# Optimization experiments

Measured on AMD Instinct MI355X. Metric: run time of the kernel, lower is better.

## Reference

```python
import jax, jax.numpy as jnp
import numpy as np

B, L, D, V, T = 4, 512, 2048, 32000, 1024


def setup_inputs() -> dict:
    key = jax.random.key(0)
    k1, k2, k3 = jax.random.split(key, 3)
    encoder_outs = jax.random.normal(k1, (B, L, D), dtype=jnp.float32)
    embed_weight = jax.random.normal(k2, (V, D), dtype=jnp.float32) * 0.02
    input_ids = jax.random.randint(k3, (B, T), 0, V)
    # encoder (audio) tokens occupy the prefix of the LLM input sequence
    modality_mask = jnp.broadcast_to(jnp.arange(T) < L, (B, T))
    return {
        "encoder_outs": encoder_outs,
        "embed_weight": embed_weight,
        "input_ids": input_ids,
        "modality_mask": modality_mask,
    }


def reference(encoder_outs, embed_weight, input_ids, modality_mask):
    # chunked matmul in torch == one big contraction: (B,L,D) x (V,D) -> (B,L,V)
    sim = jnp.einsum("bld,vd->blv", encoder_outs, embed_weight)
    enc_norm = jnp.sqrt(jnp.sum(jnp.square(encoder_outs), axis=-1, keepdims=True))
    w_norm = jnp.sqrt(jnp.sum(jnp.square(embed_weight), axis=-1))  # (V,)
    cosine = sim / enc_norm / w_norm[None, None, :]
    quantize_index = jnp.argmax(cosine, axis=-1)  # (B, L)
    enc_quant = embed_weight[quantize_index]      # (B, L, D) gather lookup

    inputs_embeds = embed_weight[input_ids]       # (B, T, D)
    # pad encoder tokens to full sequence length, then blend via modality mask
    enc_pad = jnp.pad(enc_quant, ((0, 0), (0, T - L), (0, 0)))
    blended = jnp.where(modality_mask[:, :, None], enc_pad, inputs_embeds)
    return blended, quantize_index
```

## Files before the change

### kernel.cpp

```cpp
#include <hip/hip_runtime.h>
#include <math.h>

typedef __attribute__((ext_vector_type(8))) short short8v;
typedef __attribute__((ext_vector_type(4))) float f32x4;
typedef unsigned long long u64;
typedef unsigned short ushort_t;

constexpr int Bb = 4;
constexpr int Ll = 512;
constexpr int Dk = 2048;
constexpr int Vv = 32000;
constexpr int Tt = 1024;
constexpr int Mrows = Bb * Ll;

constexpr int BM = 256;
constexpr int BN = 256;
constexpr int BK = 64;
constexpr int NKT = Dk / BK;
constexpr int NBX = Mrows / BM;
constexpr int NBY = Vv / BN;
constexpr int NWG = NBX * NBY;
constexpr int CHUNK = NWG / 8;

constexpr int KCAND = 8;
constexpr int CAND_STRIDE = 500;

constexpr int FBM = 128;
constexpr int FBN = 128;
constexpr int FNVB = Vv / FBN;

constexpr size_t WS_NEEDED = 147914752ull;

__device__ __forceinline__ unsigned int fkey(float f) {
    unsigned int u = __float_as_uint(f);
    return (u & 0x80000000u) ? ~u : (u | 0x80000000u);
}
__device__ __forceinline__ void top2(u64& b1, u64& b2, u64 p) {
    if (p > b1) { b2 = b1; b1 = p; }
    else if (p > b2) { b2 = p; }
}
__device__ __forceinline__ u64 shfl64(u64 x, int m) {
    unsigned lo = __shfl_xor((unsigned)x, m, 64);
    unsigned hi = __shfl_xor((unsigned)(x >> 32), m, 64);
    return ((u64)hi << 32) | lo;
}
__device__ __forceinline__ ushort_t bftrunc(float x) {
    return (ushort_t)(__float_as_uint(x) >> 16);
}
__device__ __forceinline__ void gload_lds16(const void* g, void* l) {
    __builtin_amdgcn_global_load_lds(
        (const __attribute__((address_space(1))) unsigned int*)g,
        (__attribute__((address_space(3))) unsigned int*)l, 16, 0, 0);
}

__global__ __launch_bounds__(256) void convertA_kernel(const float* __restrict__ A,
                                                       ushort_t* __restrict__ Ab) {
    int i = blockIdx.x * blockDim.x + threadIdx.x;
    const float4* src = (const float4*)A;
    float4 x = src[i * 2], y = src[i * 2 + 1];
    ushort_t o[8] = {bftrunc(x.x), bftrunc(x.y), bftrunc(x.z), bftrunc(x.w),
                     bftrunc(y.x), bftrunc(y.y), bftrunc(y.z), bftrunc(y.w)};
    *(int4*)(Ab + (size_t)i * 8) = *(const int4*)o;
}

__global__ __launch_bounds__(256) void convertW_kernel(const float* __restrict__ W,
                                                       ushort_t* __restrict__ Wb,
                                                       float* __restrict__ winv) {
    int wave = (blockIdx.x * blockDim.x + threadIdx.x) >> 6;
    int lane = threadIdx.x & 63;
    if (wave >= Vv) return;
    const float4* row = (const float4*)(W + (size_t)wave * Dk);
    ushort4* orow = (ushort4*)(Wb + (size_t)wave * Dk);
    float s = 0.f;
#pragma unroll
    for (int i = 0; i < Dk / 4 / 64; ++i) {
        float4 v = row[lane + 64 * i];
        s = fmaf(v.x, v.x, s); s = fmaf(v.y, v.y, s);
        s = fmaf(v.z, v.z, s); s = fmaf(v.w, v.w, s);
        ushort4 o;
        o.x = bftrunc(v.x); o.y = bftrunc(v.y);
        o.z = bftrunc(v.z); o.w = bftrunc(v.w);
        orow[lane + 64 * i] = o;
    }
#pragma unroll
    for (int off = 32; off; off >>= 1) s += __shfl_down(s, off, 64);
    if (lane == 0) winv[wave] = 1.0f / sqrtf(s);
}

__global__ __launch_bounds__(256) void wnorm_kernel(const float* __restrict__ W,
                                                    float* __restrict__ winv) {
    int wave = (blockIdx.x * blockDim.x + threadIdx.x) >> 6;
    int lane = threadIdx.x & 63;
    if (wave >= Vv) return;
    const float4* row = (const float4*)(W + (size_t)wave * Dk);
    float s = 0.f;
#pragma unroll
    for (int i = 0; i < Dk / 4 / 64; ++i) {
        float4 v = row[lane + 64 * i];
        s = fmaf(v.x, v.x, s); s = fmaf(v.y, v.y, s);
        s = fmaf(v.z, v.z, s); s = fmaf(v.w, v.w, s);
    }
#pragma unroll
    for (int off = 32; off; off >>= 1) s += __shfl_down(s, off, 64);
    if (lane == 0) winv[wave] = 1.0f / sqrtf(s);
}

__global__ void init_best_kernel(u64* __restrict__ best) {
    int i = blockIdx.x * blockDim.x + threadIdx.x;
    if (i < Mrows) best[i] = 0ull;
}

__global__ __launch_bounds__(512, 2) void score_topk_kernel(
    const ushort_t* __restrict__ Ab, const ushort_t* __restrict__ Wb,
    const float* __restrict__ winv, u64* __restrict__ cand) {
    __shared__ __align__(16) ushort_t Alds[2][16384];
    __shared__ __align__(16) ushort_t Wlds[2][16384];

    const int orig = blockIdx.x;
    const int swz = (orig & 7) * CHUNK + (orig >> 3);
    const int bx = swz & (NBX - 1);
    const int by = swz >> 3;
    const int row0 = bx * BM;
    const int v0 = by * BN;

    const int tid = threadIdx.x;
    const int lane = tid & 63;
    const int w = tid >> 6;
    const int wr = w >> 2;
    const int wc = w & 3;

    const int rsub = lane & 15;
    const int ksub = (lane >> 4) * 8;

    const ushort_t* srcA[4];
    const ushort_t* srcW[4];
#pragma unroll
    for (int q = 0; q < 4; ++q) {
        const int fb = w * 4 + q, sub = fb >> 1, kk = fb & 1;
        srcA[q] = Ab + (size_t)(row0 + sub * 16 + rsub) * Dk + kk * 32 + ksub;
        srcW[q] = Wb + (size_t)(v0 + sub * 16 + rsub) * Dk + kk * 32 + ksub;
    }

    auto stage = [&](int buf, int t) {
        const int k0 = t * BK;
#pragma unroll
        for (int q = 0; q < 4; ++q) {
            const int fb = w * 4 + q;
            gload_lds16(srcA[q] + k0, &Alds[buf][fb * 512]);
            gload_lds16(srcW[q] + k0, &Wlds[buf][fb * 512]);
        }
    };

    f32x4 acc[8][4];
#pragma unroll
    for (int i = 0; i < 8; ++i)
#pragma unroll
        for (int j = 0; j < 4; ++j) acc[i][j] = (f32x4){0.f, 0.f, 0.f, 0.f};

    stage(0, 0);
    __syncthreads();
    int cur = 0;
    for (int t = 0; t < NKT; ++t) {
        if (t + 1 < NKT) stage(cur ^ 1, t + 1);
        const short8v* Ap = (const short8v*)&Alds[cur][0];
        const short8v* Wp = (const short8v*)&Wlds[cur][0];
#pragma unroll
        for (int kk = 0; kk < 2; ++kk) {
            short8v a[8], b[4];
#pragma unroll
            for (int mf = 0; mf < 8; ++mf)
                a[mf] = Ap[((wr * 8 + mf) * 2 + kk) * 64 + lane];
#pragma unroll
            for (int nf = 0; nf < 4; ++nf)
                b[nf] = Wp[((wc * 4 + nf) * 2 + kk) * 64 + lane];
            __builtin_amdgcn_s_setprio(1);
#pragma unroll
            for (int mf = 0; mf < 8; ++mf)
#pragma unroll
                for (int nf = 0; nf < 4; ++nf)
                    acc[mf][nf] = __builtin_amdgcn_mfma_f32_16x16x32_bf16(
                        a[mf], b[nf], acc[mf][nf], 0, 0, 0);
            __builtin_amdgcn_s_setprio(0);
        }
        __syncthreads();
        cur ^= 1;
    }

    const int cb = lane & 15;
    float wv[4];
#pragma unroll
    for (int nf = 0; nf < 4; ++nf) wv[nf] = winv[v0 + wc * 64 + nf * 16 + cb];

    u64(*red)[8] = (u64(*)[8]) & Alds[0][0];
#pragma unroll
    for (int mf = 0; mf < 8; ++mf) {
#pragma unroll
        for (int reg = 0; reg < 4; ++reg) {
            u64 b1 = 0, b2 = 0;
#pragma unroll
            for (int nf = 0; nf < 4; ++nf) {
                float s = acc[mf][nf][reg] * wv[nf];
                int v = v0 + wc * 64 + nf * 16 + cb;
                u64 p = ((u64)fkey(s) << 32) | (unsigned)(Vv - 1 - v);
                top2(b1, b2, p);
            }
#pragma unroll
            for (int m = 1; m < 16; m <<= 1) {
                u64 o1 = shfl64(b1, m);
                u64 o2 = shfl64(b2, m);
                top2(b1, b2, o1);
                top2(b1, b2, o2);
            }
            if (cb == 0) {
                int rl = wr * 128 + mf * 16 + ((lane >> 4) << 2) + reg;
                red[rl][wc * 2] = b1;
                red[rl][wc * 2 + 1] = b2;
            }
        }
    }
    __syncthreads();
    if (tid < BM) {
        u64 b1 = red[tid][0], b2 = red[tid][1];
#pragma unroll
        for (int j = 2; j < 8; ++j) top2(b1, b2, red[tid][j]);
        u64* c = cand + (size_t)(row0 + tid) * CAND_STRIDE + by * 2;
        c[0] = b1;
        c[1] = b2;
    }
}

template <typename LdsT>
__device__ __forceinline__ void topk_epilogue_f(f32x4 (&acc)[4][4], LdsT* ldsbase,
                                                const float* __restrict__ winv,
                                                u64* __restrict__ cand, int row0, int v0,
                                                int vby, int tid, int lane, int wr,
                                                int wc) {
    const int cbase = v0 + wc * 64 + (lane & 15);
    float wv[4];
#pragma unroll
    for (int nf = 0; nf < 4; ++nf) wv[nf] = winv[cbase + nf * 16];

    u64(*red)[4] = (u64(*)[4])ldsbase;
#pragma unroll
    for (int mf = 0; mf < 4; ++mf) {
#pragma unroll
        for (int reg = 0; reg < 4; ++reg) {
            u64 b1 = 0, b2 = 0;
#pragma unroll
            for (int nf = 0; nf < 4; ++nf) {
                float s = acc[mf][nf][reg] * wv[nf];
                int v = cbase + nf * 16;
                u64 p = ((u64)fkey(s) << 32) | (unsigned)(Vv - 1 - v);
                top2(b1, b2, p);
            }
#pragma unroll
            for (int m = 1; m < 16; m <<= 1) {
                u64 o1 = shfl64(b1, m);
                u64 o2 = shfl64(b2, m);
                top2(b1, b2, o1);
                top2(b1, b2, o2);
            }
            if ((lane & 15) == 0) {
                int rl = wr * 64 + mf * 16 + ((lane >> 4) << 2) + reg;
                red[rl][wc * 2] = b1;
                red[rl][wc * 2 + 1] = b2;
            }
        }
    }
    __syncthreads();
    if (tid < FBM) {
        u64 b1 = red[tid][0], b2 = red[tid][1];
        top2(b1, b2, red[tid][2]);
        top2(b1, b2, red[tid][3]);
        u64* c = cand + (size_t)(row0 + tid) * CAND_STRIDE + vby * 2;
        c[0] = b1;
        c[1] = b2;
    }
}

__global__ __launch_bounds__(256) void score_topk_fallback(
    const float* __restrict__ A, const float* __restrict__ W,
    const float* __restrict__ winv, u64* __restrict__ cand) {
    __shared__ __align__(16) short Albuf[4096];
    __shared__ __align__(16) short Wlbuf[4096];

    const int tid = threadIdx.x;
    const int row0 = blockIdx.x * FBM;
    const int v0 = blockIdx.y * FBN;
    const int lane = tid & 63;
    const int wid = tid >> 6;
    const int wr = wid >> 1, wc = wid & 1;

    const int rA = ((tid >> 6) << 4) + (tid & 15);
    const int kk = ((tid >> 4) & 3) * 8;

    const float* pa = A + (size_t)(row0 + rA) * Dk + kk;
    const float* pw = W + (size_t)(v0 + rA) * Dk + kk;

    float4 fa0, fa1, fa2, fa3, fw0, fw1, fw2, fw3;
    auto ld4 = [](const float* p) { return *(const float4*)p; };
    auto load_regs = [&](int k0) {
        fa0 = ld4(pa + k0); fa1 = ld4(pa + k0 + 4);
        fa2 = ld4(pa + k0 + (size_t)64 * Dk); fa3 = ld4(pa + k0 + (size_t)64 * Dk + 4);
        fw0 = ld4(pw + k0); fw1 = ld4(pw + k0 + 4);
        fw2 = ld4(pw + k0 + (size_t)64 * Dk); fw3 = ld4(pw + k0 + (size_t)64 * Dk + 4);
    };
    auto pk = [](float lo, float hi) {
        return (int)((__float_as_uint(lo) >> 16) | (__float_as_uint(hi) & 0xFFFF0000u));
    };
    auto cv = [&](float4 a, float4 b) {
        int4 r; r.x = pk(a.x, a.y); r.y = pk(a.z, a.w);
        r.z = pk(b.x, b.y); r.w = pk(b.z, b.w); return r;
    };
    auto write_lds = [&]() {
        *(int4*)(Albuf + tid * 8) = cv(fa0, fa1);
        *(int4*)(Albuf + tid * 8 + 2048) = cv(fa2, fa3);
        *(int4*)(Wlbuf + tid * 8) = cv(fw0, fw1);
        *(int4*)(Wlbuf + tid * 8 + 2048) = cv(fw2, fw3);
    };

    f32x4 acc[4][4];
#pragma unroll
    for (int i = 0; i < 4; ++i)
#pragma unroll
        for (int j = 0; j < 4; ++j) acc[i][j] = (f32x4){0.f, 0.f, 0.f, 0.f};

    load_regs(0);
    for (int kt = 0; kt < Dk / 32; ++kt) {
        write_lds();
        __syncthreads();
        if (kt + 1 < Dk / 32) load_regs((kt + 1) * 32);
        short8v af[4], bf[4];
        const short8v* Ap = (const short8v*)Albuf;
        const short8v* Wp = (const short8v*)Wlbuf;
#pragma unroll
        for (int mf = 0; mf < 4; ++mf) af[mf] = Ap[(wr * 4 + mf) * 64 + lane];
#pragma unroll
        for (int nf = 0; nf < 4; ++nf) bf[nf] = Wp[(wc * 4 + nf) * 64 + lane];
#pragma unroll
        for (int mf = 0; mf < 4; ++mf)
#pragma unroll
            for (int nf = 0; nf < 4; ++nf)
                acc[mf][nf] = __builtin_amdgcn_mfma_f32_16x16x32_bf16(
                    af[mf], bf[nf], acc[mf][nf], 0, 0, 0);
        __syncthreads();
    }

    topk_epilogue_f(acc, Albuf, winv, cand, row0, v0, blockIdx.y, tid, lane, wr, wc);
}

__global__ __launch_bounds__(256) void topk_kernel(const u64* __restrict__ cand,
                                                   int* __restrict__ sel, int nents) {
    int row = blockIdx.x * 4 + (threadIdx.x >> 6);
    int lane = threadIdx.x & 63;
    if (row >= Mrows) return;
    const u64* c = cand + (size_t)row * CAND_STRIDE;
    u64 v[8];
#pragma unroll
    for (int i = 0; i < 8; ++i) {
        int idx = lane + i * 64;
        v[i] = (idx < nents) ? c[idx] : 0ull;
    }
#pragma unroll
    for (int it = 0; it < KCAND; ++it) {
        u64 lm = 0;
#pragma unroll
        for (int i = 0; i < 8; ++i) lm = v[i] > lm ? v[i] : lm;
#pragma unroll
        for (int m = 32; m; m >>= 1) {
            u64 o = shfl64(lm, m);
            lm = o > lm ? o : lm;
        }
#pragma unroll
        for (int i = 0; i < 8; ++i)
            if (v[i] == lm) v[i] = 0;
        if (lane == 0) sel[row * KCAND + it] = Vv - 1 - (int)(unsigned)(lm & 0xFFFFFFFFu);
    }
}

__global__ __launch_bounds__(256) void rescore_kernel(
    const float* __restrict__ A, const float* __restrict__ W,
    const float* __restrict__ winv, const int* __restrict__ sel,
    u64* __restrict__ best) {
    int gw = (int)((blockIdx.x * blockDim.x + threadIdx.x) >> 6);
    int lane = threadIdx.x & 63;
    if (gw >= Mrows * KCAND) return;
    int row = gw >> 3, c = gw & 7;
    int v = sel[row * KCAND + c];
    const float4* a = (const float4*)(A + (size_t)row * Dk);
    const float4* w = (const float4*)(W + (size_t)v * Dk);
    float s = 0.f;
#pragma unroll
    for (int i = 0; i < Dk / 4 / 64; ++i) {
        float4 x = a[lane + 64 * i], y = w[lane + 64 * i];
        s = fmaf(x.x, y.x, s); s = fmaf(x.y, y.y, s);
        s = fmaf(x.z, y.z, s); s = fmaf(x.w, y.w, s);
    }
#pragma unroll
    for (int m = 32; m; m >>= 1) s += __shfl_xor(s, m, 64);
    if (lane == 0) {
        u64 p = ((u64)fkey(s * winv[v]) << 32) | (unsigned)(Vv - 1 - v);
        atomicMax(best + row, p);
    }
}

__global__ __launch_bounds__(256) void blend_kernel(
    const float* __restrict__ emb, const int* __restrict__ ids,
    const u64* __restrict__ best, float* __restrict__ out) {
    int row = blockIdx.x;
    int b = row / Tt;
    int t = row % Tt;
    int idx;
    if (t < Ll) {
        idx = Vv - 1 - (int)(best[b * Ll + t] & 0xFFFFFFFFu);
    } else {
        idx = ids[row];
    }
    const float4* src = (const float4*)(emb + (size_t)idx * Dk);
    float4* dst = (float4*)(out + (size_t)row * Dk);
    for (int i = threadIdx.x; i < Dk / 4; i += blockDim.x) dst[i] = src[i];
    if (t < Ll && threadIdx.x == 0) {
        out[(size_t)Bb * Tt * Dk + (size_t)(b * Ll + t)] = (float)idx;
    }
}

extern "C" void kernel_launch(void* const* d_in, const int* in_sizes, int n_in,
                              void* d_out, int out_size, void* d_ws, size_t ws_size,
                              hipStream_t stream) {
    const float* encoder_outs = (const float*)d_in[0];
    const float* embed_weight = (const float*)d_in[1];
    const int* input_ids = (const int*)d_in[2];

    float* out = (float*)d_out;

    float* winv = (float*)d_ws;
    u64* best = (u64*)((char*)d_ws + 131072);
    int* sel = (int*)((char*)d_ws + 147456);
    u64* cand = (u64*)((char*)d_ws + 262144);
    ushort_t* Abf = (ushort_t*)((char*)d_ws + 8454144);
    ushort_t* Wbf = (ushort_t*)((char*)d_ws + 16842752);

    init_best_kernel<<<(Mrows + 255) / 256, 256, 0, stream>>>(best);

    if (ws_size >= WS_NEEDED) {
        convertA_kernel<<<Mrows * Dk / 8 / 256, 256, 0, stream>>>(encoder_outs, Abf);
        convertW_kernel<<<Vv * 64 / 256, 256, 0, stream>>>(embed_weight, Wbf, winv);
        score_topk_kernel<<<NWG, 512, 0, stream>>>(Abf, Wbf, winv, cand);
        topk_kernel<<<Mrows / 4, 256, 0, stream>>>(cand, sel, 2 * NBY);
    } else {
        wnorm_kernel<<<Vv * 64 / 256, 256, 0, stream>>>(embed_weight, winv);
        dim3 grid(Mrows / FBM, Vv / FBN);
        score_topk_fallback<<<grid, 256, 0, stream>>>(encoder_outs, embed_weight, winv,
                                                      cand);
        topk_kernel<<<Mrows / 4, 256, 0, stream>>>(cand, sel, 2 * FNVB);
    }
    rescore_kernel<<<Mrows * KCAND / 4, 256, 0, stream>>>(encoder_outs, embed_weight,
                                                          winv, sel, best);
    blend_kernel<<<Bb * Tt, 256, 0, stream>>>(embed_weight, input_ids, best, out);
}
```

Baseline: 1.116 ms.

## Switch score GEMM to 32x32x16 MFMA with BK=32 staging

The score/top-k GEMM kernel moves from 16x16x32 bf16 MFMAs to 32x32x16 MFMAs, with each wave computing 4x2 tiles of 32x32. The K tile is halved to 32, which halves LDS use per block and changes the global-to-LDS staging layout. The epilogue is reworked to the 32x32 accumulator layout, with a wider 32-lane shuffle reduction. Larger MFMAs need fewer LDS fragment reads per flop, but halving BK doubles the number of K iterations and barriers.

```diff
diff --git a/kernel.cpp b/kernel.cpp
--- a/kernel.cpp
+++ b/kernel.cpp
@@ -3,6 +3,7 @@
 
 typedef __attribute__((ext_vector_type(8))) short short8v;
 typedef __attribute__((ext_vector_type(4))) float f32x4;
+typedef __attribute__((ext_vector_type(16))) float f32x16;
 typedef unsigned long long u64;
 typedef unsigned short ushort_t;
 
@@ -15,7 +16,7 @@
 
 constexpr int BM = 256;
 constexpr int BN = 256;
-constexpr int BK = 64;
+constexpr int BK = 32;
 constexpr int NKT = Dk / BK;
 constexpr int NBX = Mrows / BM;
 constexpr int NBY = Vv / BN;
@@ -113,8 +114,8 @@
 __global__ __launch_bounds__(512, 2) void score_topk_kernel(
     const ushort_t* __restrict__ Ab, const ushort_t* __restrict__ Wb,
     const float* __restrict__ winv, u64* __restrict__ cand) {
-    __shared__ __align__(16) ushort_t Alds[2][16384];
-    __shared__ __align__(16) ushort_t Wlds[2][16384];
+    __shared__ __align__(16) ushort_t Alds[2][8192];
+    __shared__ __align__(16) ushort_t Wlds[2][8192];
 
     const int orig = blockIdx.x;
     const int swz = (orig & 7) * CHUNK + (orig >> 3);
@@ -128,91 +129,84 @@
     const int w = tid >> 6;
     const int wr = w >> 2;
     const int wc = w & 3;
-
-    const int rsub = lane & 15;
-    const int ksub = (lane >> 4) * 8;
-
-    const ushort_t* srcA[4];
-    const ushort_t* srcW[4];
-#pragma unroll
-    for (int q = 0; q < 4; ++q) {
-        const int fb = w * 4 + q, sub = fb >> 1, kk = fb & 1;
-        srcA[q] = Ab + (size_t)(row0 + sub * 16 + rsub) * Dk + kk * 32 + ksub;
-        srcW[q] = Wb + (size_t)(v0 + sub * 16 + rsub) * Dk + kk * 32 + ksub;
-    }
+    const int l31 = lane & 31;
+    const int l5 = lane >> 5;
+
+    const ushort_t* sA = Ab + (size_t)(row0 + w * 32 + l31) * Dk + l5 * 8;
+    const ushort_t* sW = Wb + (size_t)(v0 + w * 32 + l31) * Dk + l5 * 8;
+
+    f32x16 acc[4][2];
+#pragma unroll
+    for (int i = 0; i < 4; ++i)
+#pragma unroll
+        for (int j = 0; j < 2; ++j)
+#pragma unroll
+            for (int r = 0; r < 16; ++r) acc[i][j][r] = 0.f;
 
     auto stage = [&](int buf, int t) {
         const int k0 = t * BK;
-#pragma unroll
-        for (int q = 0; q < 4; ++q) {
-            const int fb = w * 4 + q;
-            gload_lds16(srcA[q] + k0, &Alds[buf][fb * 512]);
-            gload_lds16(srcW[q] + k0, &Wlds[buf][fb * 512]);
-        }
+        gload_lds16(sA + k0, &Alds[buf][(2 * w) * 512]);
+        gload_lds16(sA + k0 + 16, &Alds[buf][(2 * w + 1) * 512]);
+        gload_lds16(sW + k0, &Wlds[buf][(2 * w) * 512]);
+        gload_lds16(sW + k0 + 16, &Wlds[buf][(2 * w + 1) * 512]);
     };
-
-    f32x4 acc[8][4];
-#pragma unroll
-    for (int i = 0; i < 8; ++i)
-#pragma unroll
-        for (int j = 0; j < 4; ++j) acc[i][j] = (f32x4){0.f, 0.f, 0.f, 0.f};
 
     stage(0, 0);
     __syncthreads();
+
     int cur = 0;
     for (int t = 0; t < NKT; ++t) {
         if (t + 1 < NKT) stage(cur ^ 1, t + 1);
         const short8v* Ap = (const short8v*)&Alds[cur][0];
         const short8v* Wp = (const short8v*)&Wlds[cur][0];
-#pragma unroll
-        for (int kk = 0; kk < 2; ++kk) {
-            short8v a[8], b[4];
-#pragma unroll
-            for (int mf = 0; mf < 8; ++mf)
-                a[mf] = Ap[((wr * 8 + mf) * 2 + kk) * 64 + lane];
-#pragma unroll
-            for (int nf = 0; nf < 4; ++nf)
-                b[nf] = Wp[((wc * 4 + nf) * 2 + kk) * 64 + lane];
-            __builtin_amdgcn_s_setprio(1);
-#pragma unroll
-            for (int mf = 0; mf < 8; ++mf)
-#pragma unroll
-                for (int nf = 0; nf < 4; ++nf)
-                    acc[mf][nf] = __builtin_amdgcn_mfma_f32_16x16x32_bf16(
+        __builtin_amdgcn_s_setprio(1);
+#pragma unroll
+        for (int c = 0; c < 2; ++c) {
+            short8v a[4], b[2];
+#pragma unroll
+            for (int mf = 0; mf < 4; ++mf)
+                a[mf] = Ap[((wr * 4 + mf) * 2 + c) * 64 + lane];
+#pragma unroll
+            for (int nf = 0; nf < 2; ++nf)
+                b[nf] = Wp[((wc * 2 + nf) * 2 + c) * 64 + lane];
+#pragma unroll
+            for (int mf = 0; mf < 4; ++mf)
+#pragma unroll
+                for (int nf = 0; nf < 2; ++nf)
+                    acc[mf][nf] = __builtin_amdgcn_mfma_f32_32x32x16_bf16(
                         a[mf], b[nf], acc[mf][nf], 0, 0, 0);
-            __builtin_amdgcn_s_setprio(0);
         }
+        __builtin_amdgcn_s_setprio(0);
         __syncthreads();
         cur ^= 1;
     }
 
-    const int cb = lane & 15;
-    float wv[4];
-#pragma unroll
-    for (int nf = 0; nf < 4; ++nf) wv[nf] = winv[v0 + wc * 64 + nf * 16 + cb];
+    float wv[2];
+#pragma unroll
+    for (int nf = 0; nf < 2; ++nf) wv[nf] = winv[v0 + wc * 64 + nf * 32 + l31];
 
     u64(*red)[8] = (u64(*)[8]) & Alds[0][0];
 #pragma unroll
-    for (int mf = 0; mf < 8; ++mf) {
-#pragma unroll
-        for (int reg = 0; reg < 4; ++reg) {
+    for (int mf = 0; mf < 4; ++mf) {
+#pragma unroll
+        for (int reg = 0; reg < 16; ++reg) {
             u64 b1 = 0, b2 = 0;
 #pragma unroll
-            for (int nf = 0; nf < 4; ++nf) {
+            for (int nf = 0; nf < 2; ++nf) {
                 float s = acc[mf][nf][reg] * wv[nf];
-                int v = v0 + wc * 64 + nf * 16 + cb;
+                int v = v0 + wc * 64 + nf * 32 + l31;
                 u64 p = ((u64)fkey(s) << 32) | (unsigned)(Vv - 1 - v);
                 top2(b1, b2, p);
             }
 #pragma unroll
-            for (int m = 1; m < 16; m <<= 1) {
+            for (int m = 1; m < 32; m <<= 1) {
                 u64 o1 = shfl64(b1, m);
                 u64 o2 = shfl64(b2, m);
                 top2(b1, b2, o1);
                 top2(b1, b2, o2);
             }
-            if (cb == 0) {
-                int rl = wr * 128 + mf * 16 + ((lane >> 4) << 2) + reg;
+            if (l31 == 0) {
+                int rl = wr * 128 + mf * 32 + (reg & 3) + 8 * (reg >> 2) + 4 * l5;
                 red[rl][wc * 2] = b1;
                 red[rl][wc * 2 + 1] = b2;
             }
```

Measured after the change: 3.996 ms. +258.2%, slower.
